# Optimization experiments

Measured on AMD Instinct MI355X. Metric: run time of the kernel, lower is better.

## Reference

```python
import jax, jax.numpy as jnp
import numpy as np

def setup_inputs() -> dict:
    key = jax.random.key(0)
    k1, k2, k3 = jax.random.split(key, 3)
    B, NC, NQ, D = 16, 1024, 128, 512
    c_vector = jax.random.normal(k1, (B, NC, D), dtype=jnp.float32)
    q_vector = jax.random.normal(k2, (B, NQ, D), dtype=jnp.float32)
    kernel = jax.random.normal(k3, (3 * D, 1), dtype=jnp.float32) * 0.05
    bias = jnp.ones((), dtype=jnp.float32)
    return {"c_vector": c_vector, "q_vector": q_vector, "kernel": kernel, "bias": bias}

def reference(c_vector, q_vector, kernel, bias):
    # sim[b,i,j] = w . [c_i ; q_j ; c_i*q_j] + bias, decomposed to avoid the
    # (B, n_c, n_q, 3d) intermediate of the original tile+concat formulation.
    D = c_vector.shape[-1]
    w = kernel[:, 0]                      # (3d,)
    w_c, w_q, w_cq = w[:D], w[D:2 * D], w[2 * D:]
    c_term = c_vector @ w_c               # (B, n_c)
    q_term = q_vector @ w_q               # (B, n_q)
    cq_term = jnp.einsum('bid,bjd->bij', c_vector * w_cq, q_vector)  # (B, n_c, n_q)
    return cq_term + c_term[:, :, None] + q_term[:, None, :] + bias
```

## Files before the change

kernel.cpp:

```cpp
#include <hip/hip_runtime.h>
#include <hip/hip_bf16.h>

#define B_   16
#define NC_  1024
#define NQ_  128
#define D_   512
#define NKT  8

typedef __attribute__((ext_vector_type(8))) short bf16x8;
typedef __attribute__((ext_vector_type(4))) float f32x4;

__device__ __forceinline__ short f2bf(float x) {
    return __builtin_bit_cast(short, __float2bfloat16(x));
}
__device__ __forceinline__ float bf2f(short s) {
    unsigned u = ((unsigned)(unsigned short)s) << 16;
    return __builtin_bit_cast(float, u);
}

__global__ __launch_bounds__(256, 2) void sim_kernel(
    const float* __restrict__ c, const float* __restrict__ q,
    const float* __restrict__ kern, const float* __restrict__ bias_p,
    float* __restrict__ out)
{
    __shared__ __align__(16) char  lds[2][16384];
    __shared__ __align__(16) short wl[1536];
    __shared__ __align__(16) float ctl[64];

    const int bid   = blockIdx.x;
    const int b     = ((bid & 7) << 1) | (bid >> 8);
    const int inner = (bid >> 3) & 31;
    const int mt    = inner >> 1;
    const int nb    = inner & 1;
    const int tid   = threadIdx.x;
    const int lane  = tid & 63;
    const int w     = tid >> 6;
    const int wm    = w >> 1, wn = w & 1;
    const int rif   = lane & 15;
    const int kg    = lane >> 4;

    if (tid < 192) {
        const float* s = kern + tid * 8;
        f32x4 v0 = *(const f32x4*)s;
        f32x4 v1 = *(const f32x4*)(s + 4);
        bf16x8 o;
        o[0]=f2bf(v0[0]); o[1]=f2bf(v0[1]); o[2]=f2bf(v0[2]); o[3]=f2bf(v0[3]);
        o[4]=f2bf(v1[0]); o[5]=f2bf(v1[1]); o[6]=f2bf(v1[2]); o[7]=f2bf(v1[3]);
        *(bf16x8*)&wl[tid * 8] = o;
    }

    const int ar0 = tid >> 3, ar1 = ar0 + 32;
    const int acs = (tid & 7) * 8;
    const float* ag0 = c + (size_t)(b * NC_ + mt * 64 + ar0) * D_ + acs;
    const float* ag1 = c + (size_t)(b * NC_ + mt * 64 + ar1) * D_ + acs;
    const int aw0 = ar0 * 128 + ((acs * 2) ^ ((ar0 & 7) << 4));
    const int aw1 = ar1 * 128 + ((acs * 2) ^ ((ar1 & 7) << 4));

    const int bj = tid >> 2, bp = tid & 3;
    const float* bg = q + (size_t)(b * NQ_ + nb * 64 + bj) * D_ + bp * 16;
    const int bw0 = 8192 + bj * 128 + ((bp * 32)      ^ ((bj & 7) << 4));
    const int bw1 = 8192 + bj * 128 + ((bp * 32 + 16) ^ ((bj & 7) << 4));

    f32x4 sa[2][4], sb[2][4];
    float ct0 = 0.f, ct1 = 0.f;
    f32x4 acc00 = {}, acc01 = {}, acc10 = {}, acc11 = {};
    f32x4 acc_q0 = {}, acc_q1 = {};

#define ISSUE(T)                                                   \
    do { const int s_ = (T) & 1;                                   \
        sa[s_][0] = *(const f32x4*)(ag0 + (T) * 64);               \
        sa[s_][1] = *(const f32x4*)(ag0 + (T) * 64 + 4);           \
        sa[s_][2] = *(const f32x4*)(ag1 + (T) * 64);               \
        sa[s_][3] = *(const f32x4*)(ag1 + (T) * 64 + 4);           \
        sb[s_][0] = *(const f32x4*)(bg + (T) * 64);                \
        sb[s_][1] = *(const f32x4*)(bg + (T) * 64 + 4);            \
        sb[s_][2] = *(const f32x4*)(bg + (T) * 64 + 8);            \
        sb[s_][3] = *(const f32x4*)(bg + (T) * 64 + 12);           \
    } while (0)

#define WRITE(T)                                                               \
    do { const int s_ = (T) & 1; char* Lw = &lds[s_][0];                       \
        bf16x8 wcq = *(const bf16x8*)&wl[1024 + (T) * 64 + acs];               \
        bf16x8 wc8 = *(const bf16x8*)&wl[       (T) * 64 + acs];               \
        bf16x8 oa0, oa1, ob0, ob1;                                             \
        _Pragma("unroll")                                                      \
        for (int e = 0; e < 8; ++e) {                                          \
            float wcqf = bf2f(wcq[e]);                                         \
            float x0 = sa[s_][e >> 2][e & 3];                                  \
            float x1 = sa[s_][2 + (e >> 2)][e & 3];                            \
            oa0[e] = f2bf(x0 * wcqf);                                          \
            oa1[e] = f2bf(x1 * wcqf);                                          \
            float wcf = bf2f(wc8[e]);                                          \
            ct0 += x0 * wcf;  ct1 += x1 * wcf;                                 \
            ob0[e] = f2bf(sb[s_][e >> 2][e & 3]);                              \
            ob1[e] = f2bf(sb[s_][2 + (e >> 2)][e & 3]);                        \
        }                                                                      \
        *(bf16x8*)(Lw + aw0) = oa0;                                            \
        *(bf16x8*)(Lw + aw1) = oa1;                                            \
        *(bf16x8*)(Lw + bw0) = ob0;                                            \
        *(bf16x8*)(Lw + bw1) = ob1;                                            \
    } while (0)

#define COMPUTE(T)                                                                                   \
    do { const char* L = &lds[(T) & 1][0];                                                           \
        _Pragma("unroll")                                                                            \
        for (int kk = 0; kk < 2; ++kk) {                                                             \
            const int ks = kk * 64 + kg * 16;                                                        \
            bf16x8 af0, af1, bf0, bf1, wqf;                                                          \
            { int r = wm*32 + rif;      af0 = *(const bf16x8*)(L + r*128 + (ks ^ ((r & 7) << 4))); } \
            { int r = wm*32 + 16 + rif; af1 = *(const bf16x8*)(L + r*128 + (ks ^ ((r & 7) << 4))); } \
            { int j = wn*32 + rif;      bf0 = *(const bf16x8*)(L + 8192 + j*128 + (ks ^ ((j & 7) << 4))); } \
            { int j = wn*32 + 16 + rif; bf1 = *(const bf16x8*)(L + 8192 + j*128 + (ks ^ ((j & 7) << 4))); } \
            wqf = *(const bf16x8*)&wl[512 + (T) * 64 + kk * 32 + kg * 8];                            \
            acc00 = __builtin_amdgcn_mfma_f32_16x16x32_bf16(af0, bf0, acc00, 0, 0, 0);               \
            acc01 = __builtin_amdgcn_mfma_f32_16x16x32_bf16(af0, bf1, acc01, 0, 0, 0);               \
            acc10 = __builtin_amdgcn_mfma_f32_16x16x32_bf16(af1, bf0, acc10, 0, 0, 0);               \
            acc11 = __builtin_amdgcn_mfma_f32_16x16x32_bf16(af1, bf1, acc11, 0, 0, 0);               \
            acc_q0 = __builtin_amdgcn_mfma_f32_16x16x32_bf16(wqf, bf0, acc_q0, 0, 0, 0);             \
            acc_q1 = __builtin_amdgcn_mfma_f32_16x16x32_bf16(wqf, bf1, acc_q1, 0, 0, 0);             \
        }                                                                                            \
    } while (0)

    ISSUE(0); ISSUE(1);
    asm volatile("s_waitcnt lgkmcnt(0)" ::: "memory");
    __builtin_amdgcn_sched_barrier(0);
    __builtin_amdgcn_s_barrier();
    WRITE(0);
    asm volatile("s_waitcnt lgkmcnt(0)" ::: "memory");
    __builtin_amdgcn_sched_barrier(0);
    __builtin_amdgcn_s_barrier();

    #pragma unroll
    for (int kt = 0; kt < NKT; ++kt) {
        if (kt + 2 < NKT) ISSUE(kt + 2);
        __builtin_amdgcn_sched_barrier(0);
        COMPUTE(kt);
        if (kt + 1 < NKT) {
            WRITE(kt + 1);
            asm volatile("s_waitcnt lgkmcnt(0)" ::: "memory");
            __builtin_amdgcn_sched_barrier(0);
            __builtin_amdgcn_s_barrier();
        }
    }
#undef ISSUE
#undef WRITE
#undef COMPUTE

    ct0 += __shfl_xor(ct0, 1); ct0 += __shfl_xor(ct0, 2); ct0 += __shfl_xor(ct0, 4);
    ct1 += __shfl_xor(ct1, 1); ct1 += __shfl_xor(ct1, 2); ct1 += __shfl_xor(ct1, 4);
    if ((tid & 7) == 0) { ctl[ar0] = ct0; ctl[ar1] = ct1; }
    asm volatile("s_waitcnt lgkmcnt(0)" ::: "memory");
    __builtin_amdgcn_sched_barrier(0);
    __builtin_amdgcn_s_barrier();

    const float bias = *bias_p;
    const float qt0 = acc_q0[0] + bias;
    const float qt1 = acc_q1[0] + bias;
    #pragma unroll
    for (int mf = 0; mf < 2; ++mf) {
        f32x4 ctv = *(const f32x4*)&ctl[wm * 32 + mf * 16 + kg * 4];
        float* o = out + ((size_t)(b * NC_ + mt * 64 + wm * 32 + mf * 16 + kg * 4)) * NQ_
                 + nb * 64 + wn * 32 + rif;
        const f32x4 a0 = mf ? acc10 : acc00;
        const f32x4 a1 = mf ? acc11 : acc01;
        #pragma unroll
        for (int r = 0; r < 4; ++r) {
            o[(size_t)r * NQ_ +  0] = a0[r] + ctv[r] + qt0;
            o[(size_t)r * NQ_ + 16] = a1[r] + ctv[r] + qt1;
        }
    }
}

extern "C" void kernel_launch(void* const* d_in, const int* in_sizes, int n_in,
                              void* d_out, int out_size, void* d_ws, size_t ws_size,
                              hipStream_t stream) {
    const float* c    = (const float*)d_in[0];
    const float* q    = (const float*)d_in[1];
    const float* kern = (const float*)d_in[2];
    const float* bias = (const float*)d_in[3];
    float* out = (float*)d_out;

    sim_kernel<<<512, 256, 0, stream>>>(c, q, kern, bias, out);
}
```

Baseline: 16.05 us.

## Double threads per block to 512 with 8 waves each owning a 32x16 tile

Each block now runs 512 threads (8 waves in a 2x4 grid) instead of 256. Each thread loads half as much global data and each wave computes half as many MFMA tiles. The aim is more latency hiding and memory-level parallelism per CU for this small, bandwidth-bound problem. In exchange, the q-term MFMA is recomputed in more waves, each wave reuses its tile less, and launch bounds now ask for 4 blocks of 512 threads per CU, which limits registers.

```diff
diff --git a/kernel.cpp b/kernel.cpp
--- a/kernel.cpp
+++ b/kernel.cpp
@@ -18,7 +18,7 @@
     return __builtin_bit_cast(float, u);
 }
 
-__global__ __launch_bounds__(256, 2) void sim_kernel(
+__global__ __launch_bounds__(512, 4) void sim_kernel(
     const float* __restrict__ c, const float* __restrict__ q,
     const float* __restrict__ kern, const float* __restrict__ bias_p,
     float* __restrict__ out)
@@ -34,8 +34,8 @@
     const int nb    = inner & 1;
     const int tid   = threadIdx.x;
     const int lane  = tid & 63;
-    const int w     = tid >> 6;
-    const int wm    = w >> 1, wn = w & 1;
+    const int wid   = tid >> 6;
+    const int wm    = wid >> 2, wn = wid & 3;
     const int rif   = lane & 15;
     const int kg    = lane >> 4;
 
@@ -49,56 +49,42 @@
         *(bf16x8*)&wl[tid * 8] = o;
     }
 
-    const int ar0 = tid >> 3, ar1 = ar0 + 32;
+    const int ar  = tid >> 3;
     const int acs = (tid & 7) * 8;
-    const float* ag0 = c + (size_t)(b * NC_ + mt * 64 + ar0) * D_ + acs;
-    const float* ag1 = c + (size_t)(b * NC_ + mt * 64 + ar1) * D_ + acs;
-    const int aw0 = ar0 * 128 + ((acs * 2) ^ ((ar0 & 7) << 4));
-    const int aw1 = ar1 * 128 + ((acs * 2) ^ ((ar1 & 7) << 4));
+    const float* ag = c + (size_t)(b * NC_ + mt * 64 + ar) * D_ + acs;
+    const int aw = ar * 128 + ((acs * 2) ^ ((ar & 7) << 4));
 
-    const int bj = tid >> 2, bp = tid & 3;
-    const float* bg = q + (size_t)(b * NQ_ + nb * 64 + bj) * D_ + bp * 16;
-    const int bw0 = 8192 + bj * 128 + ((bp * 32)      ^ ((bj & 7) << 4));
-    const int bw1 = 8192 + bj * 128 + ((bp * 32 + 16) ^ ((bj & 7) << 4));
+    const int bj  = ar;
+    const float* bg = q + (size_t)(b * NQ_ + nb * 64 + bj) * D_ + acs;
+    const int bw = 8192 + bj * 128 + ((acs * 2) ^ ((bj & 7) << 4));
 
-    f32x4 sa[2][4], sb[2][4];
-    float ct0 = 0.f, ct1 = 0.f;
-    f32x4 acc00 = {}, acc01 = {}, acc10 = {}, acc11 = {};
-    f32x4 acc_q0 = {}, acc_q1 = {};
+    f32x4 sa[2][2], sb[2][2];
+    float cta = 0.f;
+    f32x4 acc00 = {}, acc10 = {};
+    f32x4 acc_q0 = {};
 
 #define ISSUE(T)                                                   \
     do { const int s_ = (T) & 1;                                   \
-        sa[s_][0] = *(const f32x4*)(ag0 + (T) * 64);               \
-        sa[s_][1] = *(const f32x4*)(ag0 + (T) * 64 + 4);           \
-        sa[s_][2] = *(const f32x4*)(ag1 + (T) * 64);               \
-        sa[s_][3] = *(const f32x4*)(ag1 + (T) * 64 + 4);           \
+        sa[s_][0] = *(const f32x4*)(ag + (T) * 64);                \
+        sa[s_][1] = *(const f32x4*)(ag + (T) * 64 + 4);            \
         sb[s_][0] = *(const f32x4*)(bg + (T) * 64);                \
         sb[s_][1] = *(const f32x4*)(bg + (T) * 64 + 4);            \
-        sb[s_][2] = *(const f32x4*)(bg + (T) * 64 + 8);            \
-        sb[s_][3] = *(const f32x4*)(bg + (T) * 64 + 12);           \
     } while (0)
 
 #define WRITE(T)                                                               \
     do { const int s_ = (T) & 1; char* Lw = &lds[s_][0];                       \
         bf16x8 wcq = *(const bf16x8*)&wl[1024 + (T) * 64 + acs];               \
         bf16x8 wc8 = *(const bf16x8*)&wl[       (T) * 64 + acs];               \
-        bf16x8 oa0, oa1, ob0, ob1;                                             \
+        bf16x8 oa, ob;                                                         \
         _Pragma("unroll")                                                      \
         for (int e = 0; e < 8; ++e) {                                          \
-            float wcqf = bf2f(wcq[e]);                                         \
-            float x0 = sa[s_][e >> 2][e & 3];                                  \
-            float x1 = sa[s_][2 + (e >> 2)][e & 3];                            \
-            oa0[e] = f2bf(x0 * wcqf);                                          \
-            oa1[e] = f2bf(x1 * wcqf);                                          \
-            float wcf = bf2f(wc8[e]);                                          \
-            ct0 += x0 * wcf;  ct1 += x1 * wcf;                                 \
-            ob0[e] = f2bf(sb[s_][e >> 2][e & 3]);                              \
-            ob1[e] = f2bf(sb[s_][2 + (e >> 2)][e & 3]);                        \
+            float x = sa[s_][e >> 2][e & 3];                                   \
+            oa[e] = f2bf(x * bf2f(wcq[e]));                                    \
+            cta += x * bf2f(wc8[e]);                                           \
+            ob[e] = f2bf(sb[s_][e >> 2][e & 3]);                               \
         }                                                                      \
-        *(bf16x8*)(Lw + aw0) = oa0;                                            \
-        *(bf16x8*)(Lw + aw1) = oa1;                                            \
-        *(bf16x8*)(Lw + bw0) = ob0;                                            \
-        *(bf16x8*)(Lw + bw1) = ob1;                                            \
+        *(bf16x8*)(Lw + aw) = oa;                                              \
+        *(bf16x8*)(Lw + bw) = ob;                                              \
     } while (0)
 
 #define COMPUTE(T)                                                                                   \
@@ -106,18 +92,14 @@
         _Pragma("unroll")                                                                            \
         for (int kk = 0; kk < 2; ++kk) {                                                             \
             const int ks = kk * 64 + kg * 16;                                                        \
-            bf16x8 af0, af1, bf0, bf1, wqf;                                                          \
+            bf16x8 af0, af1, bf0, wqf;                                                               \
             { int r = wm*32 + rif;      af0 = *(const bf16x8*)(L + r*128 + (ks ^ ((r & 7) << 4))); } \
             { int r = wm*32 + 16 + rif; af1 = *(const bf16x8*)(L + r*128 + (ks ^ ((r & 7) << 4))); } \
-            { int j = wn*32 + rif;      bf0 = *(const bf16x8*)(L + 8192 + j*128 + (ks ^ ((j & 7) << 4))); } \
-            { int j = wn*32 + 16 + rif; bf1 = *(const bf16x8*)(L + 8192 + j*128 + (ks ^ ((j & 7) << 4))); } \
+            { int j = wn*16 + rif;      bf0 = *(const bf16x8*)(L + 8192 + j*128 + (ks ^ ((j & 7) << 4))); } \
             wqf = *(const bf16x8*)&wl[512 + (T) * 64 + kk * 32 + kg * 8];                            \
             acc00 = __builtin_amdgcn_mfma_f32_16x16x32_bf16(af0, bf0, acc00, 0, 0, 0);               \
-            acc01 = __builtin_amdgcn_mfma_f32_16x16x32_bf16(af0, bf1, acc01, 0, 0, 0);               \
             acc10 = __builtin_amdgcn_mfma_f32_16x16x32_bf16(af1, bf0, acc10, 0, 0, 0);               \
-            acc11 = __builtin_amdgcn_mfma_f32_16x16x32_bf16(af1, bf1, acc11, 0, 0, 0);               \
             acc_q0 = __builtin_amdgcn_mfma_f32_16x16x32_bf16(wqf, bf0, acc_q0, 0, 0, 0);             \
-            acc_q1 = __builtin_amdgcn_mfma_f32_16x16x32_bf16(wqf, bf1, acc_q1, 0, 0, 0);             \
         }                                                                                            \
     } while (0)
 
@@ -146,28 +128,23 @@
 #undef WRITE
 #undef COMPUTE
 
-    ct0 += __shfl_xor(ct0, 1); ct0 += __shfl_xor(ct0, 2); ct0 += __shfl_xor(ct0, 4);
-    ct1 += __shfl_xor(ct1, 1); ct1 += __shfl_xor(ct1, 2); ct1 += __shfl_xor(ct1, 4);
-    if ((tid & 7) == 0) { ctl[ar0] = ct0; ctl[ar1] = ct1; }
+    cta += __shfl_xor(cta, 1); cta += __shfl_xor(cta, 2); cta += __shfl_xor(cta, 4);
+    if ((tid & 7) == 0) ctl[ar] = cta;
     asm volatile("s_waitcnt lgkmcnt(0)" ::: "memory");
     __builtin_amdgcn_sched_barrier(0);
     __builtin_amdgcn_s_barrier();
 
     const float bias = *bias_p;
     const float qt0 = acc_q0[0] + bias;
-    const float qt1 = acc_q1[0] + bias;
     #pragma unroll
     for (int mf = 0; mf < 2; ++mf) {
         f32x4 ctv = *(const f32x4*)&ctl[wm * 32 + mf * 16 + kg * 4];
         float* o = out + ((size_t)(b * NC_ + mt * 64 + wm * 32 + mf * 16 + kg * 4)) * NQ_
-                 + nb * 64 + wn * 32 + rif;
+                 + nb * 64 + wn * 16 + rif;
         const f32x4 a0 = mf ? acc10 : acc00;
-        const f32x4 a1 = mf ? acc11 : acc01;
         #pragma unroll
-        for (int r = 0; r < 4; ++r) {
-            o[(size_t)r * NQ_ +  0] = a0[r] + ctv[r] + qt0;
-            o[(size_t)r * NQ_ + 16] = a1[r] + ctv[r] + qt1;
-        }
+        for (int r = 0; r < 4; ++r)
+            o[(size_t)r * NQ_] = a0[r] + ctv[r] + qt0;
     }
 }
 
@@ -180,5 +157,5 @@
     const float* bias = (const float*)d_in[3];
     float* out = (float*)d_out;
 
-    sim_kernel<<<512, 256, 0, stream>>>(c, q, kern, bias, out);
+    sim_kernel<<<512, 512, 0, stream>>>(c, q, kern, bias, out);
 }
```

After: 15.20 us (median of 2 runs). -5.2%, faster.
